# Kernel tuning notes

Hardware: AMD Instinct MI355X
Metric: run time of the kernel (lower is better)

Reference implementation:

```python
import jax, jax.numpy as jnp
import numpy as np

N = 8192          # flattened seq_len*batch
HID = 1024        # hid_dim == emb_dim
VOCAB = 50257
NSAMPLED = 8192
NEG_INF = -1e37   # accidental-match fill used by the torch module


def setup_inputs() -> dict:
    key = jax.random.key(0)
    k1, k2, k3, k4, k5, k6, k7 = jax.random.split(key, 7)
    output = jax.random.normal(k1, (N, HID), dtype=jnp.float32)
    targets = jax.random.randint(k2, (N,), 0, VOCAB, dtype=jnp.int32)
    sample_ids = jax.random.randint(k3, (NSAMPLED,), 0, VOCAB, dtype=jnp.int32)
    # expected-count frequencies from the log-uniform sampler: strictly positive
    true_freq = jax.random.uniform(k4, (N,), dtype=jnp.float32, minval=1e-4, maxval=1.0)
    sample_freq = jax.random.uniform(k5, (NSAMPLED,), dtype=jnp.float32, minval=1e-4, maxval=1.0)
    weight = jax.random.normal(k6, (VOCAB, HID), dtype=jnp.float32) * 0.02
    bias = jax.random.normal(k7, (VOCAB,), dtype=jnp.float32) * 0.02
    return {"output": output, "targets": targets, "sample_ids": sample_ids,
            "true_freq": true_freq, "sample_freq": sample_freq,
            "weight": weight, "bias": bias}


def reference(output, targets, sample_ids, true_freq, sample_freq, weight, bias):
    # Gather rows for true classes and sampled classes
    true_w = weight[targets]          # (N, HID)
    true_b = bias[targets]            # (N,)
    sample_w = weight[sample_ids]     # (NSAMPLED, HID)
    sample_b = bias[sample_ids]       # (NSAMPLED,)

    # Per-row dot with true class row + bias
    true_logits = jnp.sum(output * true_w, axis=1) + true_b          # (N,)
    # Dense GEMM against sampled rows + bias
    sample_logits = jnp.einsum('nh,sh->ns', output, sample_w) + sample_b  # (N, NSAMPLED)

    # remove_accidental_match: mask out sampled ids equal to the true target
    acc = targets[:, None] == sample_ids[None, :]                    # (N, NSAMPLED)
    sample_logits = jnp.where(acc, NEG_INF, sample_logits)

    # log-uniform sampling correction (subtract log expected counts)
    true_logits = true_logits - jnp.log(true_freq)
    sample_logits = sample_logits - jnp.log(sample_freq)[None, :]

    logits = jnp.concatenate([true_logits[:, None], sample_logits], axis=1)  # (N, NSAMPLED+1)
    new_targets = jnp.zeros((output.shape[0],), dtype=jnp.int32)
    return logits, new_targets
```

## Files before the change

kernel.cpp:

```cpp
#include <hip/hip_runtime.h>

#define NROWS 8192
#define HID   1024
#define NSAMP 8192
#define LCOLS 8193
#define NEG_INF_F (-1e37f)

#define SCALE_A 127
#define SCALE_B 122

typedef __attribute__((ext_vector_type(4)))  int   i32x4;
typedef __attribute__((ext_vector_type(8)))  int   i32x8;
typedef __attribute__((ext_vector_type(4)))  float f32x4;
typedef __attribute__((ext_vector_type(16))) float f32x16;
typedef f32x4 __attribute__((aligned(4))) f32x4u;
typedef __attribute__((ext_vector_type(8))) __bf16 bf16x8;
typedef __attribute__((ext_vector_type(8))) unsigned short u16x8;

__device__ __forceinline__ unsigned short f2bf(float x) {
  unsigned u = __float_as_uint(x);
  u += 0x7fffu + ((u >> 16) & 1u);
  return (unsigned short)(u >> 16);
}

#define GLOAD_LDS16(g, l)                                                      \
  __builtin_amdgcn_global_load_lds(                                            \
      (const __attribute__((address_space(1))) void*)(g),                      \
      (__attribute__((address_space(3))) void*)(l), 16, 0, 0)


__device__ __forceinline__ unsigned fp4nib(float x) {
  unsigned s = (__float_as_uint(x) >> 31) << 3;
  float y = fabsf(x);
  unsigned n = y < 0.25f ? 0u : y < 0.75f ? 1u : y < 1.25f ? 2u :
               y < 1.75f ? 3u : y < 2.5f  ? 4u : y < 3.5f  ? 5u :
               y < 5.0f  ? 6u : 7u;
  return n | s;
}

__device__ __forceinline__ unsigned long long pk16(const float* e, float m) {
  unsigned long long r = 0;
  #pragma unroll
  for (int i = 0; i < 8; ++i) {
    unsigned long long b =
        fp4nib(e[2 * i] * m) | (fp4nib(e[2 * i + 1] * m) << 4);
    r |= b << (8 * i);
  }
  return r;
}

__global__ void k_prep(const float* __restrict__ A, const float* __restrict__ W,
                       const int* __restrict__ sid, const int* __restrict__ tgt,
                       const float* __restrict__ bias, const float* __restrict__ tfreq,
                       unsigned char* __restrict__ Ab, unsigned char* __restrict__ Bb,
                       float* __restrict__ out) {
  const int bid = blockIdx.x;
  if (bid < 4096) {
    const bool isA = bid < 2048;
    const int t = (isA ? bid : bid - 2048) * 256 + threadIdx.x;
    const int BI = t >> 7;
    const int l = (t & 127) >> 1;
    const int j0 = (t & 1) * 16;
    const int row = (BI >> 4) * 32 + (l & 31);
    const int k0 = (BI & 15) * 64 + (l >> 5) * 32 + j0;
    const float* src = isA ? (A + (size_t)row * HID + k0)
                           : (W + (size_t)sid[row] * HID + k0);
    float e[16];
    #pragma unroll
    for (int v = 0; v < 4; ++v) {
      float4 f = ((const float4*)src)[v];
      e[v * 4 + 0] = f.x; e[v * 4 + 1] = f.y; e[v * 4 + 2] = f.z; e[v * 4 + 3] = f.w;
    }
    unsigned long long r = pk16(e, isA ? 1.0f : 32.0f);
    ((unsigned long long*)(isA ? Ab : Bb))[t] = r;
  } else {
    const int n = (bid - 4096) * 4 + (threadIdx.x >> 6);
    const int l = threadIdx.x & 63;
    const int tg = tgt[n];
    float4 a = ((const float4*)(A + (size_t)n * HID))[l];
    float4 wv = ((const float4*)(W + (size_t)tg * HID))[l];
    float p = a.x * wv.x + a.y * wv.y + a.z * wv.z + a.w * wv.w;
    #pragma unroll
    for (int off = 32; off > 0; off >>= 1) p += __shfl_down(p, off);
    if (l == 0) {
      out[(size_t)n * LCOLS] = p + bias[tg] - __logf(tfreq[n]);
      ((int*)out)[(size_t)NROWS * LCOLS + n] = 0;
    }
  }
}

__global__ __launch_bounds__(256, 4)
void k_gemm4(const unsigned char* __restrict__ Ab, const unsigned char* __restrict__ Bb,
             const int* __restrict__ tgt, const int* __restrict__ sid,
             const float* __restrict__ bias, const float* __restrict__ sfreq,
             float* __restrict__ out) {
  __shared__ unsigned char lds[32768];
  const int t = threadIdx.x, w = t >> 6, l = t & 63;

  const int orig = blockIdx.y * 64 + blockIdx.x;
  const int c = orig & 7, q = orig >> 3;
  const int mi = (c >> 1) * 16 + (q >> 5);
  const int ni = (c & 1) * 32 + (q & 31);
  const int m0 = mi * 128, n0 = ni * 128;
  const int wm = w >> 1, wn = w & 1;
  f32x16 acc[2][2] = {};

  const unsigned char* gA = Ab + ((size_t)(mi * 4 + w) * 16) * 1024 + l * 16;
  const unsigned char* gB = Bb + ((size_t)(ni * 4 + w) * 16) * 1024 + l * 16;

#define STAGE(buf_, KK_)                                                       \
  do {                                                                         \
    unsigned char* _d = lds + (buf_) * 8192 + w * 1024;                        \
    GLOAD_LDS16(gA + (KK_) * 1024, _d);                                        \
    GLOAD_LDS16(gB + (KK_) * 1024, _d + 4096);                                 \
  } while (0)

  STAGE(0, 0);
  asm volatile("s_waitcnt vmcnt(0)" ::: "memory");
  __builtin_amdgcn_s_barrier();

  int buf = 0;
  for (int KK = 0; KK < 16; ++KK) {
    if (KK < 15) STAGE(buf ^ 1, KK + 1);
    __builtin_amdgcn_sched_barrier(0);

    const unsigned char* sAb = lds + buf * 8192;
    const unsigned char* sBb = sAb + 4096;
    i32x4 aF[2], bF[2];
    #pragma unroll
    for (int mf = 0; mf < 2; ++mf)
      aF[mf] = *(const i32x4*)&sAb[(wm * 2 + mf) * 1024 + l * 16];
    #pragma unroll
    for (int nf = 0; nf < 2; ++nf)
      bF[nf] = *(const i32x4*)&sBb[(wn * 2 + nf) * 1024 + l * 16];
    __builtin_amdgcn_sched_barrier(0);

    __builtin_amdgcn_s_setprio(1);
    #pragma unroll
    for (int mf = 0; mf < 2; ++mf) {
      const i32x8 af = (i32x8){aF[mf][0], aF[mf][1], aF[mf][2], aF[mf][3],
                               0, 0, 0, 0};
      #pragma unroll
      for (int nf = 0; nf < 2; ++nf) {
        const i32x8 bf = (i32x8){bF[nf][0], bF[nf][1], bF[nf][2], bF[nf][3],
                                 0, 0, 0, 0};
        acc[mf][nf] = __builtin_amdgcn_mfma_scale_f32_32x32x64_f8f6f4(
            af, bf, acc[mf][nf], 4, 4, 0, SCALE_A, 0, SCALE_B);
      }
    }
    __builtin_amdgcn_s_setprio(0);

    asm volatile("s_waitcnt vmcnt(0)" ::: "memory");
    __builtin_amdgcn_s_barrier();
    buf ^= 1;
  }
#undef STAGE

  float* tile = (float*)lds;
  #pragma unroll
  for (int half = 0; half < 2; ++half) {
    if (half) __syncthreads();
    if (wm == half) {
      #pragma unroll
      for (int nf = 0; nf < 2; ++nf) {
        const int col = wn * 64 + nf * 32 + (l & 31);
        const int gcol = n0 + col;
        const int sv = sid[gcol];
        const float sbv = bias[sv] - __logf(sfreq[gcol]);
        #pragma unroll
        for (int mf = 0; mf < 2; ++mf) {
          #pragma unroll
          for (int i = 0; i < 16; ++i) {
            const int r = mf * 32 + (i & 3) + 8 * (i >> 2) + 4 * (l >> 5);
            float cv = acc[mf][nf][i] + sbv;
            if (tgt[m0 + half * 64 + r] == sv) cv = NEG_INF_F;
            tile[r * 128 + (col ^ ((r & 4) << 2))] = cv;
          }
        }
      }
    }
    __syncthreads();
    #pragma unroll
    for (int p = 0; p < 8; ++p) {
      const int idx = p * 256 + t;
      const int r = idx >> 5;
      const int c16 = idx & 31;
      f32x4 v = *(const f32x4*)&tile[r * 128 + ((c16 * 4) ^ ((r & 4) << 2))];
      __builtin_nontemporal_store(
          v, (f32x4u*)&out[(size_t)(m0 + half * 64 + r) * LCOLS + 1 + n0 + c16 * 4]);
    }
  }
}

__device__ __forceinline__ void pack8(unsigned short* p, float4 a, float4 b) {
  u16x8 v;
  v[0] = f2bf(a.x); v[1] = f2bf(a.y); v[2] = f2bf(a.z); v[3] = f2bf(a.w);
  v[4] = f2bf(b.x); v[5] = f2bf(b.y); v[6] = f2bf(b.z); v[7] = f2bf(b.w);
  *(u16x8*)p = v;
}

__global__ void k_true_fb(const float* __restrict__ X, const int* __restrict__ tgt,
                          const float* __restrict__ W, const float* __restrict__ bias,
                          const float* __restrict__ tfreq, float* __restrict__ out) {
  const int n = blockIdx.x * 4 + (threadIdx.x >> 6);
  const int l = threadIdx.x & 63;
  const int tg = tgt[n];
  float4 a = ((const float4*)(X + (size_t)n * HID))[l];
  float4 wv = ((const float4*)(W + (size_t)tg * HID))[l];
  float p = a.x * wv.x + a.y * wv.y + a.z * wv.z + a.w * wv.w;
  #pragma unroll
  for (int off = 32; off > 0; off >>= 1) p += __shfl_down(p, off);
  if (l == 0) {
    out[(size_t)n * LCOLS] = p + bias[tg] - __logf(tfreq[n]);
    ((int*)out)[(size_t)NROWS * LCOLS + n] = 0;
  }
}

__global__ __launch_bounds__(256)
void k_gemm_fb(const float* __restrict__ Af, const float* __restrict__ W,
               const int* __restrict__ tgt, const int* __restrict__ sid,
               const float* __restrict__ bias, const float* __restrict__ sfreq,
               float* __restrict__ out) {
  __shared__ unsigned short sA[128 * 32];
  __shared__ unsigned short sB[128 * 32];
  const int t = threadIdx.x;
  const int w = t >> 6, l = t & 63;
  const int m0 = blockIdx.y * 128, n0 = blockIdx.x * 128;
  const int wm = w >> 1, wn = w & 1;
  f32x4 acc[4][4] = {};
  const int srow = w * 16 + (l >> 2);
  const int scol = (l & 3) * 8;

  const int id0 = sid[n0 + srow], id1 = sid[n0 + 64 + srow];
  const float* gaf0 = Af + (size_t)(m0 + srow) * HID + scol;
  const float* gaf1 = gaf0 + (size_t)64 * HID;
  const float* gbf0 = W + (size_t)id0 * HID + scol;
  const float* gbf1 = W + (size_t)id1 * HID + scol;
  for (int kk = 0; kk < HID; kk += 32) {
    float4 a0 = *(const float4*)(gaf0 + kk), a1 = *(const float4*)(gaf0 + kk + 4);
    float4 a2 = *(const float4*)(gaf1 + kk), a3 = *(const float4*)(gaf1 + kk + 4);
    float4 b0 = *(const float4*)(gbf0 + kk), b1 = *(const float4*)(gbf0 + kk + 4);
    float4 b2 = *(const float4*)(gbf1 + kk), b3 = *(const float4*)(gbf1 + kk + 4);
    __syncthreads();
    pack8(&sA[t * 8], a0, a1);
    pack8(&sA[2048 + t * 8], a2, a3);
    pack8(&sB[t * 8], b0, b1);
    pack8(&sB[2048 + t * 8], b2, b3);
    __syncthreads();
    bf16x8 af_[4], bf_[4];
    const int rl_ = l & 15, kq_ = l >> 4;
    #pragma unroll
    for (int m = 0; m < 4; m++)
      af_[m] = *(const bf16x8*)&sA[(wm * 64 + m * 16 + rl_) * 32 + kq_ * 8];
    #pragma unroll
    for (int n = 0; n < 4; n++)
      bf_[n] = *(const bf16x8*)&sB[(wn * 64 + n * 16 + rl_) * 32 + kq_ * 8];
    #pragma unroll
    for (int m = 0; m < 4; m++)
      #pragma unroll
      for (int n = 0; n < 4; n++)
        acc[m][n] = __builtin_amdgcn_mfma_f32_16x16x32_bf16(af_[m], bf_[n],
                                                            acc[m][n], 0, 0, 0);
  }
  const int rl = l & 15, rq = l >> 4;
  #pragma unroll
  for (int n = 0; n < 4; ++n) {
    const int col = n0 + wn * 64 + n * 16 + rl;
    const int sv = sid[col];
    const float sbv = bias[sv] - __logf(sfreq[col]);
    #pragma unroll
    for (int m = 0; m < 4; ++m) {
      const int rbase = m0 + wm * 64 + m * 16 + rq * 4;
      #pragma unroll
      for (int i = 0; i < 4; ++i) {
        const int r = rbase + i;
        float c = acc[m][n][i] + sbv;
        if (tgt[r] == sv) c = NEG_INF_F;
        out[(size_t)r * LCOLS + 1 + col] = c;
      }
    }
  }
}

extern "C" void kernel_launch(void* const* d_in, const int* in_sizes, int n_in,
                              void* d_out, int out_size, void* d_ws, size_t ws_size,
                              hipStream_t stream) {
  (void)in_sizes; (void)n_in; (void)out_size;
  const float* output      = (const float*)d_in[0];
  const int*   targets     = (const int*)d_in[1];
  const int*   sample_ids  = (const int*)d_in[2];
  const float* true_freq   = (const float*)d_in[3];
  const float* sample_freq = (const float*)d_in[4];
  const float* weight      = (const float*)d_in[5];
  const float* bias        = (const float*)d_in[6];
  float* out = (float*)d_out;

  const size_t needA = (size_t)NROWS * HID / 2;
  const size_t needB = (size_t)NSAMP * HID / 2;
  const bool use_ws = ws_size >= (needA + needB);

  dim3 grid(NSAMP / 128, NROWS / 128);
  if (use_ws) {
    unsigned char* Ab = (unsigned char*)d_ws;
    unsigned char* Bb = Ab + needA;
    k_prep<<<6144, 256, 0, stream>>>(output, weight, sample_ids, targets, bias,
                                     true_freq, Ab, Bb, out);
    k_gemm4<<<grid, 256, 0, stream>>>(Ab, Bb, targets, sample_ids, bias,
                                      sample_freq, out);
  } else {
    k_true_fb<<<NROWS / 4, 256, 0, stream>>>(output, targets, weight, bias,
                                             true_freq, out);
    k_gemm_fb<<<grid, 256, 0, stream>>>(output, weight, targets, sample_ids,
                                        bias, sample_freq, out);
  }
}
```

Measured before the change: 120.5 us.

## Fuse true-logit dot into A quantization and widen GEMM tile to 128x256

The prep kernel now reads each activation row once, computing the true-class dot product and packing it to FP4 in the same pass. This drops the separate true-logit blocks that re-read the activations, and prep uses non-temporal loads. The GEMM moves to 512-thread blocks covering 128x256 output tiles. Warps 0-3 stage two B fragments each and warps 4-7 stage A, and the epilogue writes out in four 32-row chunks. Larger tiles cut redundant A reloads, but fewer blocks may leave the GPU less well filled.

```diff
diff --git a/kernel.cpp b/kernel.cpp
--- a/kernel.cpp
+++ b/kernel.cpp
@@ -55,41 +55,55 @@
                        unsigned char* __restrict__ Ab, unsigned char* __restrict__ Bb,
                        float* __restrict__ out) {
   const int bid = blockIdx.x;
-  if (bid < 4096) {
-    const bool isA = bid < 2048;
-    const int t = (isA ? bid : bid - 2048) * 256 + threadIdx.x;
+  if (bid < 1024) {
+    const int row = bid * 8 + (threadIdx.x >> 5);
+    const int l32 = threadIdx.x & 31;
+    const int kb = l32 * 32;
+    const int tg = tgt[row];
+    const f32x4* pa = (const f32x4*)(A + (size_t)row * HID + kb);
+    const f32x4* pw = (const f32x4*)(W + (size_t)tg * HID + kb);
+    float e[32];
+    float dot = 0.f;
+    #pragma unroll
+    for (int v = 0; v < 8; ++v) {
+      f32x4 fa = __builtin_nontemporal_load(&pa[v]);
+      f32x4 fw = __builtin_nontemporal_load(&pw[v]);
+      e[v * 4 + 0] = fa[0]; e[v * 4 + 1] = fa[1];
+      e[v * 4 + 2] = fa[2]; e[v * 4 + 3] = fa[3];
+      dot += fa[0] * fw[0] + fa[1] * fw[1] + fa[2] * fw[2] + fa[3] * fw[3];
+    }
+    unsigned long long lo = pk16(e, 1.0f), hi = pk16(e + 16, 1.0f);
+    const size_t off = ((size_t)(row >> 5) * 16 + (l32 >> 1)) * 1024 +
+                       ((l32 & 1) * 32 + (row & 31)) * 16;
+    ulonglong2 v2; v2.x = lo; v2.y = hi;
+    *(ulonglong2*)(Ab + off) = v2;
+    #pragma unroll
+    for (int o = 16; o > 0; o >>= 1) dot += __shfl_down(dot, o, 32);
+    if (l32 == 0) {
+      out[(size_t)row * LCOLS] = dot + bias[tg] - __logf(tfreq[row]);
+      ((int*)out)[(size_t)NROWS * LCOLS + row] = 0;
+    }
+  } else {
+    const int t = (bid - 1024) * 256 + threadIdx.x;
     const int BI = t >> 7;
     const int l = (t & 127) >> 1;
     const int j0 = (t & 1) * 16;
     const int row = (BI >> 4) * 32 + (l & 31);
+    const int id = sid[row];
     const int k0 = (BI & 15) * 64 + (l >> 5) * 32 + j0;
-    const float* src = isA ? (A + (size_t)row * HID + k0)
-                           : (W + (size_t)sid[row] * HID + k0);
+    const f32x4* src = (const f32x4*)(W + (size_t)id * HID + k0);
     float e[16];
     #pragma unroll
     for (int v = 0; v < 4; ++v) {
-      float4 f = ((const float4*)src)[v];
-      e[v * 4 + 0] = f.x; e[v * 4 + 1] = f.y; e[v * 4 + 2] = f.z; e[v * 4 + 3] = f.w;
-    }
-    unsigned long long r = pk16(e, isA ? 1.0f : 32.0f);
-    ((unsigned long long*)(isA ? Ab : Bb))[t] = r;
-  } else {
-    const int n = (bid - 4096) * 4 + (threadIdx.x >> 6);
-    const int l = threadIdx.x & 63;
-    const int tg = tgt[n];
-    float4 a = ((const float4*)(A + (size_t)n * HID))[l];
-    float4 wv = ((const float4*)(W + (size_t)tg * HID))[l];
-    float p = a.x * wv.x + a.y * wv.y + a.z * wv.z + a.w * wv.w;
-    #pragma unroll
-    for (int off = 32; off > 0; off >>= 1) p += __shfl_down(p, off);
-    if (l == 0) {
-      out[(size_t)n * LCOLS] = p + bias[tg] - __logf(tfreq[n]);
-      ((int*)out)[(size_t)NROWS * LCOLS + n] = 0;
-    }
-  }
-}
-
-__global__ __launch_bounds__(256, 4)
+      f32x4 f = __builtin_nontemporal_load(&src[v]);
+      e[v * 4 + 0] = f[0]; e[v * 4 + 1] = f[1];
+      e[v * 4 + 2] = f[2]; e[v * 4 + 3] = f[3];
+    }
+    ((unsigned long long*)Bb)[t] = pk16(e, 32.0f);
+  }
+}
+
+__global__ __launch_bounds__(512, 4)
 void k_gemm4(const unsigned char* __restrict__ Ab, const unsigned char* __restrict__ Bb,
              const int* __restrict__ tgt, const int* __restrict__ sid,
              const float* __restrict__ bias, const float* __restrict__ sfreq,
@@ -97,22 +111,26 @@
   __shared__ unsigned char lds[32768];
   const int t = threadIdx.x, w = t >> 6, l = t & 63;
 
-  const int orig = blockIdx.y * 64 + blockIdx.x;
+  const int orig = blockIdx.y * 32 + blockIdx.x;
   const int c = orig & 7, q = orig >> 3;
-  const int mi = (c >> 1) * 16 + (q >> 5);
-  const int ni = (c & 1) * 32 + (q & 31);
-  const int m0 = mi * 128, n0 = ni * 128;
-  const int wm = w >> 1, wn = w & 1;
+  const int mi = (c >> 1) * 16 + (q >> 4);
+  const int ni = (c & 1) * 16 + (q & 15);
+  const int m0 = mi * 128, n0 = ni * 256;
+  const int wm = w >> 2, wn = w & 3;
   f32x16 acc[2][2] = {};
 
-  const unsigned char* gA = Ab + ((size_t)(mi * 4 + w) * 16) * 1024 + l * 16;
-  const unsigned char* gB = Bb + ((size_t)(ni * 4 + w) * 16) * 1024 + l * 16;
+  const unsigned char* gB0 = Bb + ((size_t)(ni * 8 + 2 * w) * 16) * 1024 + l * 16;
+  const unsigned char* gA0 = Ab + ((size_t)(mi * 4 + (w - 4)) * 16) * 1024 + l * 16;
 
 #define STAGE(buf_, KK_)                                                       \
   do {                                                                         \
-    unsigned char* _d = lds + (buf_) * 8192 + w * 1024;                        \
-    GLOAD_LDS16(gA + (KK_) * 1024, _d);                                        \
-    GLOAD_LDS16(gB + (KK_) * 1024, _d + 4096);                                 \
+    unsigned char* _b = lds + (buf_) * 12288;                                  \
+    if (w < 4) {                                                               \
+      GLOAD_LDS16(gB0 + (KK_) * 1024,         _b + 4096 + (2 * w) * 1024);     \
+      GLOAD_LDS16(gB0 + 16384 + (KK_) * 1024, _b + 4096 + (2 * w + 1) * 1024); \
+    } else {                                                                   \
+      GLOAD_LDS16(gA0 + (KK_) * 1024, _b + (w - 4) * 1024);                    \
+    }                                                                          \
   } while (0)
 
   STAGE(0, 0);
@@ -124,7 +142,7 @@
     if (KK < 15) STAGE(buf ^ 1, KK + 1);
     __builtin_amdgcn_sched_barrier(0);
 
-    const unsigned char* sAb = lds + buf * 8192;
+    const unsigned char* sAb = lds + buf * 12288;
     const unsigned char* sBb = sAb + 4096;
     i32x4 aF[2], bF[2];
     #pragma unroll
@@ -158,9 +176,10 @@
 
   float* tile = (float*)lds;
   #pragma unroll
-  for (int half = 0; half < 2; ++half) {
-    if (half) __syncthreads();
-    if (wm == half) {
+  for (int chunk = 0; chunk < 4; ++chunk) {
+    if (chunk) __syncthreads();
+    if (wm == (chunk >> 1)) {
+      const int mf = chunk & 1;
       #pragma unroll
       for (int nf = 0; nf < 2; ++nf) {
         const int col = wn * 64 + nf * 32 + (l & 31);
@@ -168,26 +187,23 @@
         const int sv = sid[gcol];
         const float sbv = bias[sv] - __logf(sfreq[gcol]);
         #pragma unroll
-        for (int mf = 0; mf < 2; ++mf) {
-          #pragma unroll
-          for (int i = 0; i < 16; ++i) {
-            const int r = mf * 32 + (i & 3) + 8 * (i >> 2) + 4 * (l >> 5);
-            float cv = acc[mf][nf][i] + sbv;
-            if (tgt[m0 + half * 64 + r] == sv) cv = NEG_INF_F;
-            tile[r * 128 + (col ^ ((r & 4) << 2))] = cv;
-          }
+        for (int i = 0; i < 16; ++i) {
+          const int r = (i & 3) + 8 * (i >> 2) + 4 * (l >> 5);
+          float cv = acc[mf][nf][i] + sbv;
+          if (tgt[m0 + chunk * 32 + r] == sv) cv = NEG_INF_F;
+          tile[r * 256 + (col ^ ((r & 4) << 2))] = cv;
         }
       }
     }
     __syncthreads();
     #pragma unroll
-    for (int p = 0; p < 8; ++p) {
-      const int idx = p * 256 + t;
-      const int r = idx >> 5;
-      const int c16 = idx & 31;
-      f32x4 v = *(const f32x4*)&tile[r * 128 + ((c16 * 4) ^ ((r & 4) << 2))];
+    for (int p = 0; p < 4; ++p) {
+      const int idx = p * 512 + t;
+      const int r = idx >> 6;
+      const int c16 = idx & 63;
+      f32x4 v = *(const f32x4*)&tile[r * 256 + ((c16 * 4) ^ ((r & 4) << 2))];
       __builtin_nontemporal_store(
-          v, (f32x4u*)&out[(size_t)(m0 + half * 64 + r) * LCOLS + 1 + n0 + c16 * 4]);
+          v, (f32x4u*)&out[(size_t)(m0 + chunk * 32 + r) * LCOLS + 1 + n0 + c16 * 4]);
     }
   }
 }
@@ -299,17 +315,18 @@
   const size_t needB = (size_t)NSAMP * HID / 2;
   const bool use_ws = ws_size >= (needA + needB);
 
-  dim3 grid(NSAMP / 128, NROWS / 128);
   if (use_ws) {
     unsigned char* Ab = (unsigned char*)d_ws;
     unsigned char* Bb = Ab + needA;
-    k_prep<<<6144, 256, 0, stream>>>(output, weight, sample_ids, targets, bias,
+    k_prep<<<3072, 256, 0, stream>>>(output, weight, sample_ids, targets, bias,
                                      true_freq, Ab, Bb, out);
-    k_gemm4<<<grid, 256, 0, stream>>>(Ab, Bb, targets, sample_ids, bias,
+    dim3 grid(NSAMP / 256, NROWS / 128);
+    k_gemm4<<<grid, 512, 0, stream>>>(Ab, Bb, targets, sample_ids, bias,
                                       sample_freq, out);
   } else {
     k_true_fb<<<NROWS / 4, 256, 0, stream>>>(output, targets, weight, bias,
                                              true_freq, out);
+    dim3 grid(NSAMP / 128, NROWS / 128);
     k_gemm_fb<<<grid, 256, 0, stream>>>(output, weight, targets, sample_ids,
                                         bias, sample_freq, out);
   }
```

Result: slower. 392.6 us (+225.9%).
